# Performance work log

Hardware: AMD Instinct MI355X
Metric: run time of the kernel (lower is better)

Reference implementation:

```python
import jax, jax.numpy as jnp
import numpy as np

B, C_IN, H, W = 32, 64, 64, 64
D, O, S_SP, K = 256, 512, 4, 3


def setup_inputs() -> dict:
    key = jax.random.key(0)
    k1, k2, k3, k4, k5 = jax.random.split(key, 5)
    x = jax.random.normal(k1, (B, C_IN, H, W), dtype=jnp.float32)
    dictionary = jax.random.normal(k2, (D, C_IN, K, K), dtype=jnp.float32)
    lookup_coefficients = jax.random.normal(k3, (O, S_SP), dtype=jnp.float32)
    bias = jax.random.normal(k4, (O,), dtype=jnp.float32)
    lookup_indices = jax.random.randint(k5, (O, S_SP), 0, D)
    return {
        "x": x,
        "dictionary": dictionary,
        "lookup_coefficients": lookup_coefficients,
        "bias": bias,
        "lookup_indices": lookup_indices,
    }


def reference(x, dictionary, lookup_coefficients, bias, lookup_indices):
    # Dictionary conv: S has shape [B, D, H, W] (stride 1, padding 1, 3x3 kernel)
    S = jax.lax.conv_general_dilated(
        x, dictionary,
        window_strides=(1, 1),
        padding=((1, 1), (1, 1)),
        dimension_numbers=("NCHW", "OIHW", "NCHW"),
    )
    # Build dense [O, D] combine matrix via scatter-add (duplicate indices
    # accumulate, matching the original += loop), then one GEMM.
    rows = jnp.arange(O)[:, None]  # [O, 1] broadcast against [O, sparsity]
    Wc = jnp.zeros((O, D), dtype=S.dtype).at[rows, lookup_indices].add(lookup_coefficients)
    out = jnp.einsum("bdhw,od->bohw", S, Wc)
    return out + bias[None, :, None, None]
```

## Files before the change

kernel.cpp:

```cpp
#include <hip/hip_runtime.h>
#include <stdint.h>

#define NB 32
#define NC 64
#define NH 64
#define NW 64
#define NO 512
#define HP 66

typedef __bf16 bf16x8 __attribute__((ext_vector_type(8)));
typedef short  s16x8  __attribute__((ext_vector_type(8)));
typedef float  f32x4  __attribute__((ext_vector_type(4)));

__device__ __forceinline__ uint16_t f2bf(float f) {
  uint32_t u = __builtin_bit_cast(uint32_t, f);
  u += 0x7fffu + ((u >> 16) & 1u);
  return (uint16_t)(u >> 16);
}

__device__ __forceinline__ void gld16(const uint16_t* g, uint16_t* l) {
  __builtin_amdgcn_global_load_lds(
      (const __attribute__((address_space(1))) void*)(g),
      (__attribute__((address_space(3))) void*)(l), 16, 0, 0);
}

__global__ void k_build_w(const float* __restrict__ dict,
                          const float* __restrict__ coef,
                          const int*   __restrict__ idx,
                          uint16_t*    __restrict__ Wl) {
  __shared__ float tmp[576];
  const int o = blockIdx.x;
  const int t = threadIdx.x;
  float v = 0.f;
#pragma unroll
  for (int s = 0; s < 4; ++s)
    v += coef[o * 4 + s] * dict[idx[o * 4 + s] * 576 + t];
  tmp[t] = v;
  __syncthreads();
  const int c = t & 63, p = t >> 6;
  const int sl = ((p * NO + o) * 8 + ((c >> 3) ^ (o & 7))) * 8 + (c & 7);
  Wl[sl] = f2bf(tmp[c * 9 + p]);
}

__global__ void k_nhwc(const float* __restrict__ x, uint16_t* __restrict__ xh) {
  const int bh = blockIdx.x;
  const int b = bh / HP, hp = bh % HP;
  const int t = threadIdx.x;
  uint16_t* row = xh + (size_t)(b * HP + hp) * 4096;
  if (hp == 0 || hp == HP - 1) {
    int4* r4 = reinterpret_cast<int4*>(row);
    r4[t]       = int4{0, 0, 0, 0};
    r4[t + 256] = int4{0, 0, 0, 0};
    return;
  }
  __shared__ float tile[64][65];
  const int h = hp - 1;
  const int w = t & 63;
#pragma unroll
  for (int c = (t >> 6); c < 64; c += 4)
    tile[c][w] = x[((size_t)(b * NC + c) * NH + h) * NW + w];
  __syncthreads();
#pragma unroll
  for (int i = 0; i < 2; ++i) {
    const int s = t + i * 256;
    const int w2 = s >> 3, cb = s & 7;
    uint32_t d[4];
#pragma unroll
    for (int j = 0; j < 4; ++j) {
      const uint32_t lo = f2bf(tile[cb * 8 + 2 * j][w2]);
      const uint32_t hi = f2bf(tile[cb * 8 + 2 * j + 1][w2]);
      d[j] = lo | (hi << 16);
    }
    reinterpret_cast<int4*>(row)[w2 * 8 + (cb ^ (w2 & 7))] =
        int4{(int)d[0], (int)d[1], (int)d[2], (int)d[3]};
  }
}

__global__ __launch_bounds__(512, 2) void k_conv(
    const uint16_t* __restrict__ xh,
    const uint16_t* __restrict__ Wl,
    const float*    __restrict__ bias,
    float*          __restrict__ out) {
  __shared__ __align__(16) uint16_t xs[10 * 66 * 64];
  __shared__ __align__(16) uint16_t as[3 * 128 * 64];

  const int t = threadIdx.x;
  const int flat = blockIdx.x;
  const int s    = (flat & 7) * 128 + (flat >> 3);
  const int ot   = s & 3;
  const int gy   = s >> 2;
  const int o0 = ot * 128;
  const int b  = gy >> 3;
  const int h0 = (gy & 7) * 8;

  const int lane = t & 63;
  const int wid  = t >> 6;

  if (t < 160) {
    const int r = t >> 4, sl = (t >> 3) & 1, j = t & 7;
    reinterpret_cast<int4*>(xs)[r * 528 + sl * 520 + j] = int4{0, 0, 0, 0};
  }

  {
    const uint16_t* srow = xh + (size_t)(b * HP + h0 + wid) * 4096;
    uint16_t* drow = xs + wid * 4224 + 64;
#pragma unroll
    for (int k = 0; k < 8; ++k)
      gld16(srow + k * 512 + lane * 8, drow + k * 512);
    const int r2 = 8 + (wid >> 2);
    const int kb = (wid & 3) * 2;
    const uint16_t* srow2 = xh + (size_t)(b * HP + h0 + r2) * 4096;
    uint16_t* drow2 = xs + r2 * 4224 + 64;
    gld16(srow2 + kb * 512 + lane * 8, drow2 + kb * 512);
    gld16(srow2 + (kb + 1) * 512 + lane * 8, drow2 + (kb + 1) * 512);
  }

  auto stage_a = [&](int g) {
#pragma unroll
    for (int j = 0; j < 6; ++j) {
      const int c = wid * 6 + j;
      const int tap = c >> 4, k = c & 15;
      const uint16_t* src =
          Wl + (size_t)(tap * 3 + g) * 32768 + o0 * 64 + k * 512;
      gld16(src + lane * 8, as + tap * 8192 + k * 512);
    }
  };
  stage_a(0);

  const int wm  = wid & 1;
  const int wn  = wid >> 1;
  const int l15 = lane & 15;
  const int lg  = lane >> 4;

  f32x4 acc[4][8] = {};

  __syncthreads();

#pragma unroll
  for (int g = 0; g < 3; ++g) {
    const int dw = g - 1;

#pragma unroll
    for (int q = 0; q < 2; ++q) {
      const int cbB = (q * 4 + lg) ^ ((l15 + dw) & 7);
      bf16x8 braw[4][4];
#pragma unroll
      for (int rr = 0; rr < 4; ++rr) {
        const uint16_t* rb =
            xs + (wn * 2 + rr) * 4224 + (l15 + dw + 1) * 64 + cbB * 8;
#pragma unroll
        for (int nw = 0; nw < 4; ++nw)
          braw[rr][nw] = __builtin_bit_cast(bf16x8,
              *reinterpret_cast<const s16x8*>(rb + nw * 1024));
      }
#pragma unroll
      for (int dh = 0; dh < 3; ++dh) {
        bf16x8 af[4];
#pragma unroll
        for (int m = 0; m < 4; ++m) {
          const int orow = wm * 64 + m * 16 + l15;
          const int cb = (q * 4 + lg) ^ (orow & 7);
          af[m] = __builtin_bit_cast(bf16x8,
              *reinterpret_cast<const s16x8*>(as + dh * 8192 + orow * 64 + cb * 8));
        }
#pragma unroll
        for (int m = 0; m < 4; ++m)
#pragma unroll
          for (int n = 0; n < 8; ++n)
            acc[m][n] = __builtin_amdgcn_mfma_f32_16x16x32_bf16(
                af[m], braw[(n >> 2) + dh][n & 3], acc[m][n], 0, 0, 0);
      }
    }

    if (g < 2) {
      __syncthreads();
      stage_a(g + 1);
      __syncthreads();
    }
  }

  __syncthreads();
  float* tb = reinterpret_cast<float*>(xs) + wid * 2048;
  const int hb = h0 + wn * 2;
#pragma unroll
  for (int m = 0; m < 4; ++m) {
#pragma unroll
    for (int n = 0; n < 8; ++n) {
      const int pix = (n >> 2) * 64 + (n & 3) * 16 + l15;
#pragma unroll
      for (int rr = 0; rr < 4; ++rr)
        tb[(lg * 4 + rr) * 128 + pix] = acc[m][n][rr];
    }
#pragma unroll
    for (int j = 0; j < 8; ++j) {
      const int r  = j * 64 + lane;
      const int op = r >> 5;
      const int px = (r & 31) * 4;
      f32x4 v = reinterpret_cast<f32x4*>(tb)[r];
      const int o = o0 + wm * 64 + m * 16 + op;
      const float bv = bias[o];
      v[0] += bv; v[1] += bv; v[2] += bv; v[3] += bv;
      float* dst = out +
          ((size_t)(b * NO + o) * NH + hb + (px >> 6)) * NW + (px & 63);
      __builtin_nontemporal_store(v, reinterpret_cast<f32x4*>(dst));
    }
  }
}

extern "C" void kernel_launch(void* const* d_in, const int* in_sizes, int n_in,
                              void* d_out, int out_size, void* d_ws, size_t ws_size,
                              hipStream_t stream) {
  const float* x    = (const float*)d_in[0];
  const float* dict = (const float*)d_in[1];
  const float* coef = (const float*)d_in[2];
  const float* bias = (const float*)d_in[3];
  const int*   idx  = (const int*)d_in[4];
  float* out = (float*)d_out;

  uint16_t* xh = (uint16_t*)d_ws;
  uint16_t* Wl = (uint16_t*)((char*)d_ws + (18u << 20));

  hipLaunchKernelGGL(k_build_w, dim3(NO), dim3(576), 0, stream, dict, coef, idx, Wl);
  hipLaunchKernelGGL(k_nhwc, dim3(NB * HP), dim3(256), 0, stream, x, xh);
  hipLaunchKernelGGL(k_conv, dim3(1024), dim3(512), 0, stream, xh, Wl, bias, out);
}
```

Before: 115.7 us.

## Loop all output-channel tiles per block to reuse staged input rows

Each block now loops over all four 128-channel output tiles instead of handling one, so the haloed input tile is loaded into LDS once and reused, and the grid shrinks from 1024 to 256 blocks. MFMA operands are swapped so each lane's accumulators hold 4 consecutive pixels of one channel, which lets results be stored straight from registers with the bias added and no LDS transpose. The next tile's weight stage is issued before the current tile's stores, B fragments are loaded incrementally, and setprio/barriers are added around the MFMA bursts. The cost is 256 blocks on a GPU with 256 CUs, leaving one block per CU, plus more barriers.

```diff
diff --git a/kernel.cpp b/kernel.cpp
--- a/kernel.cpp
+++ b/kernel.cpp
@@ -85,11 +85,8 @@
   __shared__ __align__(16) uint16_t as[3 * 128 * 64];
 
   const int t = threadIdx.x;
-  const int flat = blockIdx.x;
-  const int s    = (flat & 7) * 128 + (flat >> 3);
-  const int ot   = s & 3;
-  const int gy   = s >> 2;
-  const int o0 = ot * 128;
+  const int blk = blockIdx.x;
+  const int gy = (blk & 7) * 32 + (blk >> 3);
   const int b  = gy >> 3;
   const int h0 = (gy & 7) * 8;
 
@@ -115,94 +112,113 @@
     gld16(srow2 + (kb + 1) * 512 + lane * 8, drow2 + (kb + 1) * 512);
   }
 
-  auto stage_a = [&](int g) {
+  auto stage_a = [&](int otp, int g) {
+    const int oo = otp * 128;
 #pragma unroll
     for (int j = 0; j < 6; ++j) {
       const int c = wid * 6 + j;
       const int tap = c >> 4, k = c & 15;
       const uint16_t* src =
-          Wl + (size_t)(tap * 3 + g) * 32768 + o0 * 64 + k * 512;
+          Wl + (size_t)(tap * 3 + g) * 32768 + oo * 64 + k * 512;
       gld16(src + lane * 8, as + tap * 8192 + k * 512);
     }
   };
-  stage_a(0);
+  stage_a(0, 0);
 
   const int wm  = wid & 1;
   const int wn  = wid >> 1;
   const int l15 = lane & 15;
   const int lg  = lane >> 4;
 
-  f32x4 acc[4][8] = {};
-
   __syncthreads();
 
-#pragma unroll
-  for (int g = 0; g < 3; ++g) {
-    const int dw = g - 1;
-
-#pragma unroll
-    for (int q = 0; q < 2; ++q) {
-      const int cbB = (q * 4 + lg) ^ ((l15 + dw) & 7);
-      bf16x8 braw[4][4];
-#pragma unroll
-      for (int rr = 0; rr < 4; ++rr) {
-        const uint16_t* rb =
-            xs + (wn * 2 + rr) * 4224 + (l15 + dw + 1) * 64 + cbB * 8;
-#pragma unroll
-        for (int nw = 0; nw < 4; ++nw)
-          braw[rr][nw] = __builtin_bit_cast(bf16x8,
-              *reinterpret_cast<const s16x8*>(rb + nw * 1024));
+  for (int ot = 0; ot < 4; ++ot) {
+    const int o0 = ot * 128;
+    f32x4 acc[8][4];
+#pragma unroll
+    for (int pb = 0; pb < 8; ++pb)
+#pragma unroll
+      for (int ob = 0; ob < 4; ++ob)
+        acc[pb][ob] = (f32x4){0.f, 0.f, 0.f, 0.f};
+    float bvv[4];
+#pragma unroll
+    for (int ob = 0; ob < 4; ++ob)
+      bvv[ob] = bias[o0 + wm * 64 + ob * 16 + l15];
+
+#pragma unroll
+    for (int g = 0; g < 3; ++g) {
+      const int dw = g - 1;
+#pragma unroll
+      for (int q = 0; q < 2; ++q) {
+        const int cbB = (q * 4 + lg) ^ ((l15 + dw) & 7);
+        const uint16_t* xb = xs + (l15 + dw + 1) * 64 + cbB * 8;
+        const int cbA = (q * 4 + lg) ^ (l15 & 7);
+        const uint16_t* ab = as + (wm * 64 + l15) * 64 + cbA * 8;
+        bf16x8 braw[4][4];
+#pragma unroll
+        for (int dh = 0; dh < 3; ++dh) {
+          if (dh == 0) {
+#pragma unroll
+            for (int r = 0; r < 2; ++r)
+#pragma unroll
+              for (int nw = 0; nw < 4; ++nw)
+                braw[r][nw] = __builtin_bit_cast(bf16x8,
+                    *reinterpret_cast<const s16x8*>(
+                        xb + (wn * 2 + r) * 4224 + nw * 1024));
+          } else {
+            const int r = dh + 1;
+#pragma unroll
+            for (int nw = 0; nw < 4; ++nw)
+              braw[r][nw] = __builtin_bit_cast(bf16x8,
+                  *reinterpret_cast<const s16x8*>(
+                      xb + (wn * 2 + r) * 4224 + nw * 1024));
+          }
+          bf16x8 af[4];
+#pragma unroll
+          for (int ob = 0; ob < 4; ++ob)
+            af[ob] = __builtin_bit_cast(bf16x8,
+                *reinterpret_cast<const s16x8*>(ab + dh * 8192 + ob * 1024));
+          __builtin_amdgcn_s_setprio(1);
+#pragma unroll
+          for (int pb = 0; pb < 8; ++pb)
+#pragma unroll
+            for (int ob = 0; ob < 4; ++ob)
+              acc[pb][ob] = __builtin_amdgcn_mfma_f32_16x16x32_bf16(
+                  braw[(pb >> 2) + dh][pb & 3], af[ob], acc[pb][ob], 0, 0, 0);
+          __builtin_amdgcn_s_setprio(0);
+          __builtin_amdgcn_s_barrier();
+        }
       }
-#pragma unroll
-      for (int dh = 0; dh < 3; ++dh) {
-        bf16x8 af[4];
-#pragma unroll
-        for (int m = 0; m < 4; ++m) {
-          const int orow = wm * 64 + m * 16 + l15;
-          const int cb = (q * 4 + lg) ^ (orow & 7);
-          af[m] = __builtin_bit_cast(bf16x8,
-              *reinterpret_cast<const s16x8*>(as + dh * 8192 + orow * 64 + cb * 8));
-        }
-#pragma unroll
-        for (int m = 0; m < 4; ++m)
-#pragma unroll
-          for (int n = 0; n < 8; ++n)
-            acc[m][n] = __builtin_amdgcn_mfma_f32_16x16x32_bf16(
-                af[m], braw[(n >> 2) + dh][n & 3], acc[m][n], 0, 0, 0);
+      if (g < 2) {
+        asm volatile("s_waitcnt lgkmcnt(0)" ::: "memory");
+        __builtin_amdgcn_s_barrier();
+        stage_a(ot, g + 1);
+        __syncthreads();
       }
     }
 
-    if (g < 2) {
-      __syncthreads();
-      stage_a(g + 1);
-      __syncthreads();
-    }
-  }
-
-  __syncthreads();
-  float* tb = reinterpret_cast<float*>(xs) + wid * 2048;
-  const int hb = h0 + wn * 2;
-#pragma unroll
-  for (int m = 0; m < 4; ++m) {
-#pragma unroll
-    for (int n = 0; n < 8; ++n) {
-      const int pix = (n >> 2) * 64 + (n & 3) * 16 + l15;
-#pragma unroll
-      for (int rr = 0; rr < 4; ++rr)
-        tb[(lg * 4 + rr) * 128 + pix] = acc[m][n][rr];
-    }
-#pragma unroll
-    for (int j = 0; j < 8; ++j) {
-      const int r  = j * 64 + lane;
-      const int op = r >> 5;
-      const int px = (r & 31) * 4;
-      f32x4 v = reinterpret_cast<f32x4*>(tb)[r];
-      const int o = o0 + wm * 64 + m * 16 + op;
-      const float bv = bias[o];
-      v[0] += bv; v[1] += bv; v[2] += bv; v[3] += bv;
-      float* dst = out +
-          ((size_t)(b * NO + o) * NH + hb + (px >> 6)) * NW + (px & 63);
-      __builtin_nontemporal_store(v, reinterpret_cast<f32x4*>(dst));
+    asm volatile("s_waitcnt lgkmcnt(0)" ::: "memory");
+    __builtin_amdgcn_s_barrier();
+    if (ot < 3) stage_a(ot + 1, 0);
+    asm volatile("" ::: "memory");
+    const int hb = h0 + wn * 2;
+#pragma unroll
+    for (int pb = 0; pb < 8; ++pb) {
+#pragma unroll
+      for (int ob = 0; ob < 4; ++ob) {
+        const int o = o0 + wm * 64 + ob * 16 + l15;
+        f32x4 v = acc[pb][ob];
+        const float bv = bvv[ob];
+        v[0] += bv; v[1] += bv; v[2] += bv; v[3] += bv;
+        float* dst = out +
+            ((size_t)(b * NO + o) * NH + hb + (pb >> 2)) * NW +
+            (pb & 3) * 16 + lg * 4;
+        __builtin_nontemporal_store(v, reinterpret_cast<f32x4*>(dst));
+      }
+    }
+    if (ot < 3) {
+      asm volatile("s_waitcnt vmcnt(32)" ::: "memory");
+      __builtin_amdgcn_s_barrier();
     }
   }
 }
@@ -222,5 +238,5 @@
 
   hipLaunchKernelGGL(k_build_w, dim3(NO), dim3(576), 0, stream, dict, coef, idx, Wl);
   hipLaunchKernelGGL(k_nhwc, dim3(NB * HP), dim3(256), 0, stream, x, xh);
-  hipLaunchKernelGGL(k_conv, dim3(1024), dim3(512), 0, stream, xh, Wl, bias, out);
-}
+  hipLaunchKernelGGL(k_conv, dim3(256), dim3(512), 0, stream, xh, Wl, bias, out);
+}
```

New measurement: 148.7 us. 28.6% more time.
